# Performance work log

Hardware: AMD Instinct MI355X
Metric: run time of the kernel (lower is better)

## Reference

```python
import jax, jax.numpy as jnp
import numpy as np

# Static multi-level feature-map shapes (H, W) per level.
SPATIAL_SHAPES = np.array([[92, 160], [46, 80], [23, 40], [12, 20]], dtype=np.int32)
NUM_HEADS = 8
NUM_LEVELS = 4
NUM_POINTS = 4      # sampling points per head per level (num_all_points)
NUM_Z = 4           # num_Z_anchors; NUM_POINTS % NUM_Z == 0
EMBED = 256
HEAD_DIM = EMBED // NUM_HEADS


def setup_inputs() -> dict:
    key = jax.random.key(0)
    ks = jax.random.split(key, 10)
    bs, nq = 2, 10000
    nv = int((SPATIAL_SHAPES[:, 0] * SPATIAL_SHAPES[:, 1]).sum())  # 19560
    query = jax.random.normal(ks[0], (bs, nq, EMBED), jnp.float32)
    value = jax.random.normal(ks[1], (bs, nv, EMBED), jnp.float32)
    query_pos = jax.random.normal(ks[2], (bs, nq, EMBED), jnp.float32)
    reference_points = jax.random.uniform(ks[3], (bs, nq, NUM_Z, 2), jnp.float32)
    W_val = jax.random.normal(ks[4], (EMBED, EMBED), jnp.float32) / jnp.sqrt(EMBED)
    b_val = jnp.zeros((EMBED,), jnp.float32)
    W_off = jax.random.normal(ks[5], (EMBED, NUM_HEADS * NUM_LEVELS * NUM_POINTS * 2), jnp.float32) * 0.01
    b_off = jax.random.normal(ks[6], (NUM_HEADS * NUM_LEVELS * NUM_POINTS * 2,), jnp.float32) * 0.5
    W_attn = jax.random.normal(ks[7], (EMBED, NUM_HEADS * NUM_LEVELS * NUM_POINTS), jnp.float32) * 0.02
    b_attn = jnp.zeros((NUM_HEADS * NUM_LEVELS * NUM_POINTS,), jnp.float32)
    spatial_shapes = jnp.asarray(SPATIAL_SHAPES)
    return {
        'query': query, 'value': value, 'query_pos': query_pos,
        'reference_points': reference_points,
        'W_val': W_val, 'b_val': b_val, 'W_off': W_off, 'b_off': b_off,
        'W_attn': W_attn, 'b_attn': b_attn, 'spatial_shapes': spatial_shapes,
    }


def _bilinear(v, x, y, H, W):
    """grid_sample(mode='bilinear', padding_mode='zeros', align_corners=False).

    v: (bs, H, W, heads, d); x, y: (bs, nq, heads, P) pixel coords.
    Returns (bs, nq, heads, P, d).
    """
    x0 = jnp.floor(x)
    y0 = jnp.floor(y)
    wx1 = x - x0
    wy1 = y - y0
    wx0 = 1.0 - wx1
    wy0 = 1.0 - wy1
    x0i = x0.astype(jnp.int32)
    y0i = y0.astype(jnp.int32)
    b = jnp.arange(v.shape[0])[:, None, None, None]
    h = jnp.arange(v.shape[3])[None, None, :, None]

    def gather(yi, xi):
        valid = (yi >= 0) & (yi < H) & (xi >= 0) & (xi < W)
        yc = jnp.clip(yi, 0, H - 1)
        xc = jnp.clip(xi, 0, W - 1)
        g = v[b, yc, xc, h]  # (bs, nq, heads, P, d)
        return g * valid[..., None].astype(v.dtype)

    return (gather(y0i, x0i) * (wy0 * wx0)[..., None]
            + gather(y0i, x0i + 1) * (wy0 * wx1)[..., None]
            + gather(y0i + 1, x0i) * (wy1 * wx0)[..., None]
            + gather(y0i + 1, x0i + 1) * (wy1 * wx1)[..., None])


def reference(query, value, query_pos, reference_points, W_val, b_val,
              W_off, b_off, W_attn, b_attn, spatial_shapes):
    bs, nq, _ = query.shape
    q = query + query_pos
    # value projection -> per-head values
    v = (value @ W_val + b_val).reshape(bs, -1, NUM_HEADS, HEAD_DIM)
    # sampling offsets and attention weights from query
    off = (q @ W_off + b_off).reshape(bs, nq, NUM_HEADS, NUM_LEVELS, NUM_POINTS, 2)
    attn = (q @ W_attn + b_attn).reshape(bs, nq, NUM_HEADS, NUM_LEVELS * NUM_POINTS)
    attn = jax.nn.softmax(attn, axis=-1).reshape(bs, nq, NUM_HEADS, NUM_LEVELS, NUM_POINTS)
    # normalize offsets by (w, h) of each level
    norm = jnp.stack([spatial_shapes[:, 1], spatial_shapes[:, 0]], -1).astype(q.dtype)  # (L, 2)
    off = off / norm[None, None, None, :, None, :]
    # fold Z-anchor reference points in, matching the shape[-1]==2 branch
    off = off.reshape(bs, nq, NUM_HEADS, NUM_LEVELS, NUM_POINTS // NUM_Z, NUM_Z, 2)
    loc = reference_points[:, :, None, None, None, :, :] + off
    loc = loc.reshape(bs, nq, NUM_HEADS, NUM_LEVELS, NUM_POINTS, 2)
    grid = 2.0 * loc - 1.0  # grid_sample convention

    start = 0
    sampled = []
    for lvl in range(NUM_LEVELS):
        H, W = int(SPATIAL_SHAPES[lvl, 0]), int(SPATIAL_SHAPES[lvl, 1])
        vl = v[:, start:start + H * W].reshape(bs, H, W, NUM_HEADS, HEAD_DIM)
        start += H * W
        # align_corners=False pixel coords
        x = ((grid[:, :, :, lvl, :, 0] + 1.0) * W - 1.0) * 0.5
        y = ((grid[:, :, :, lvl, :, 1] + 1.0) * H - 1.0) * 0.5
        sampled.append(_bilinear(vl, x, y, H, W))
    samp = jnp.stack(sampled, axis=3)  # (bs, nq, heads, L, P, d)
    out = (samp * attn[..., None]).sum(axis=(3, 4))  # (bs, nq, heads, d)
    return out.reshape(bs, nq, NUM_HEADS * HEAD_DIM)
```

## Files before the change

kernel.cpp:

```cpp
#include <hip/hip_runtime.h>
#include <hip/hip_fp16.h>

#define NQ 10000
#define BS 2
#define NV 19560
#define NH 8
#define HD 32
#define EMB 256

typedef __attribute__((ext_vector_type(8))) short bf16x8;
typedef __attribute__((ext_vector_type(8))) unsigned short u16x8;
typedef __attribute__((ext_vector_type(4))) float f32x4;
typedef __attribute__((ext_vector_type(4))) short s16x4;

__device__ __forceinline__ unsigned short f2bf(float x) {
    unsigned u = __float_as_uint(x);
    u += 0x7FFFu + ((u >> 16) & 1u);
    return (unsigned short)(u >> 16);
}

__global__ __launch_bounds__(256) void convert_W(
    const float* __restrict__ Wv, const float* __restrict__ Wo,
    const float* __restrict__ Wa, const float* __restrict__ bv,
    const float* __restrict__ bo, const float* __restrict__ ba,
    ushort* __restrict__ Bt, float* __restrict__ bias) {
    int n = blockIdx.x;
    int k = threadIdx.x;
    float x;
    if (n < 256)       x = Wv[k * 256 + n];
    else if (n < 512)  x = Wo[k * 256 + (n - 256)];
    else               x = Wa[k * 128 + (n - 512)];
    Bt[n * 256 + k] = f2bf(x);
    if (k == 0)
        bias[n] = (n < 256) ? bv[n] : (n < 512) ? bo[n - 256] : ba[n - 512];
}

__global__ __launch_bounds__(256) void gemm_fused(
    const float* __restrict__ value, const float* __restrict__ query,
    const float* __restrict__ qpos, const ushort* __restrict__ Bt,
    const float* __restrict__ bias,
    ushort* __restrict__ Cv, float* __restrict__ C0, float* __restrict__ C1)
{
    __shared__ short As[64][40], Bhs[128][40];

    const int tid = threadIdx.x;

    const int bid0 = blockIdx.x;
    int bid;
    if (bid0 < 1224) {
        bid = (bid0 & 7) * 153 + (bid0 >> 3);
    } else {
        int q = bid0 - 1224;
        int xcd = q & 7, idx = q >> 3;
        int orig = (xcd < 3) ? (xcd * 118 + idx)
                             : (3 * 118 + (xcd - 3) * 117 + idx);
        bid = 1224 + orig;
    }

    bool isval; int mblk, npan;
    if (bid < 1224) { isval = true;  mblk = bid >> 1; npan = bid & 1; }
    else { int q = bid - 1224; isval = false; mblk = q / 3; npan = q % 3; }

    const int M  = isval ? (BS * NV) : (BS * NQ);
    const int m0 = mblk * 64;
    const int n0 = npan * 128;
    const int nbase = (isval ? 0 : 256) + n0;

    const float* A = isval ? value : query;

    const int arow = tid >> 2;
    const int acol = (tid & 3) * 8;
    const bool aval = (m0 + arow) < M;
    const float* Ap  = A    + (size_t)(m0 + arow) * 256 + acol;
    const float* A2p = qpos + (size_t)(m0 + arow) * 256 + acol;
    const int brow = tid >> 1;
    const int bcol = (tid & 1) * 16;
    const ushort* Bp = Bt + (size_t)(nbase + brow) * 256 + bcol;

    const int lane = tid & 63, wave = tid >> 6;
    const int wrow = (wave >> 1) * 32, wcol = (wave & 1) * 64;
    const int lr = lane & 15, quad = lane >> 4, lk = quad * 8;

    f32x4 acc[2][4] = {};

    for (int k0 = 0; k0 < 256; k0 += 32) {
        #pragma unroll
        for (int g = 0; g < 2; g++) {
            f32x4 v = {};
            if (aval) {
                v = *(const f32x4*)(Ap + k0 + g * 4);
                if (!isval) v += *(const f32x4*)(A2p + k0 + g * 4);
            }
            s16x4 hh;
            #pragma unroll
            for (int e = 0; e < 4; e++) hh[e] = (short)f2bf(v[e]);
            *(s16x4*)&As[arow][acol + g * 4] = hh;
        }
        *(bf16x8*)&Bhs[brow][bcol]     = *(const bf16x8*)(Bp + k0);
        *(bf16x8*)&Bhs[brow][bcol + 8] = *(const bf16x8*)(Bp + k0 + 8);
        __syncthreads();

        bf16x8 af[2], bhf[4];
        #pragma unroll
        for (int i = 0; i < 2; i++)
            af[i] = *(const bf16x8*)&As[wrow + i * 16 + lr][lk];
        #pragma unroll
        for (int j = 0; j < 4; j++)
            bhf[j] = *(const bf16x8*)&Bhs[wcol + j * 16 + lr][lk];
        #pragma unroll
        for (int i = 0; i < 2; i++)
            #pragma unroll
            for (int j = 0; j < 4; j++)
                acc[i][j] = __builtin_amdgcn_mfma_f32_16x16x32_bf16(af[i], bhf[j], acc[i][j], 0, 0, 0);
        __syncthreads();
    }

    #pragma unroll
    for (int j = 0; j < 4; j++) {
        int cc = wcol + j * 16 + lr;
        int col = n0 + cc;
        float bb = bias[nbase + cc];
        #pragma unroll
        for (int i = 0; i < 2; i++) {
            int gmb = m0 + wrow + i * 16 + quad * 4;
            #pragma unroll
            for (int r = 0; r < 4; r++) {
                int gm = gmb + r;
                if (gm < M) {
                    float val = acc[i][j][r] + bb;
                    if (isval) {
                        int h = col >> 5, d = col & 31;
                        int b = (gm >= NV) ? 1 : 0;
                        int pix = gm - b * NV;
                        Cv[((size_t)(b * 8 + h) * NV + pix) * 32 + d] =
                            __half_as_ushort(__float2half(val));
                    } else {
                        if (col < 256) C0[(size_t)gm * 256 + col] = val;
                        else           C1[(size_t)gm * 128 + (col - 256)] = val;
                    }
                }
            }
        }
    }
}

__global__ __launch_bounds__(256) void sample4(
    const ushort* __restrict__ v, const float* __restrict__ off,
    const float* __restrict__ attn, const float* __restrict__ refp,
    float* __restrict__ out)
{
    __shared__ int2 s_ow[64][65];

    const int t = threadIdx.x;
    const int combo = blockIdx.x & 15;
    const int qgrp  = blockIdx.x >> 4;
    const int b  = combo & 1;
    const int h0 = combo >> 1;

    const int q = t >> 2;
    const int l = t & 3;
    const int qt = qgrp * 64 + q;
    const bool valid = qt < NQ;
    const size_t bq = (size_t)b * NQ + (valid ? qt : NQ - 1);

    {
        f32x4 lg = *(const f32x4*)(attn + bq * 128 + h0 * 16 + l * 4);
        float mx = fmaxf(fmaxf(lg[0], lg[1]), fmaxf(lg[2], lg[3]));
        mx = fmaxf(mx, __shfl_xor(mx, 1, 4));
        mx = fmaxf(mx, __shfl_xor(mx, 2, 4));
        float e0 = __expf(lg[0] - mx), e1 = __expf(lg[1] - mx);
        float e2 = __expf(lg[2] - mx), e3 = __expf(lg[3] - mx);
        float s = e0 + e1 + e2 + e3;
        s += __shfl_xor(s, 1, 4);
        s += __shfl_xor(s, 2, 4);
        float inv = 1.f / s;

        const float Wl = (l == 0) ? 160.f : (l == 1) ? 80.f : (l == 2) ? 40.f : 20.f;
        const float Hl = (l == 0) ? 92.f  : (l == 1) ? 46.f : (l == 2) ? 23.f : 12.f;
        const int  stl = (l == 0) ? 0 : (l == 1) ? 14720 : (l == 2) ? 18400 : 19320;
        const int  Wi_ = (int)Wl, Hi_ = (int)Hl;
        const int base = ((b * 8 + h0) * NV + stl) * 32;

        f32x4 of0 = *(const f32x4*)(off + bq * 256 + h0 * 32 + l * 8);
        f32x4 of1 = *(const f32x4*)(off + bq * 256 + h0 * 32 + l * 8 + 4);
        f32x4 r0  = *(const f32x4*)(refp + bq * 8);
        f32x4 r1  = *(const f32x4*)(refp + bq * 8 + 4);

        float ws[4]  = {e0 * inv, e1 * inv, e2 * inv, e3 * inv};
        float oxs[4] = {of0[0], of0[2], of1[0], of1[2]};
        float oys[4] = {of0[1], of0[3], of1[1], of1[3]};
        float rxs[4] = {r0[0], r0[2], r1[0], r1[2]};
        float rys[4] = {r0[1], r0[3], r1[1], r1[3]};

        #pragma unroll
        for (int p = 0; p < 4; p++) {
            float x = rxs[p] * Wl + oxs[p] - 0.5f;
            float y = rys[p] * Hl + oys[p] - 0.5f;
            float x0f = floorf(x), y0f = floorf(y);
            float wx1 = x - x0f, wy1 = y - y0f;
            float wx0 = 1.f - wx1, wy0 = 1.f - wy1;
            int x0 = (int)x0f, y0 = (int)y0f;
            float mx0 = ((unsigned)x0       < (unsigned)Wi_) ? 1.f : 0.f;
            float mx1 = ((unsigned)(x0 + 1) < (unsigned)Wi_) ? 1.f : 0.f;
            float my0 = ((unsigned)y0       < (unsigned)Hi_) ? 1.f : 0.f;
            float my1 = ((unsigned)(y0 + 1) < (unsigned)Hi_) ? 1.f : 0.f;
            int xc0 = min(max(x0, 0), Wi_ - 1);
            int xc1 = min(max(x0 + 1, 0), Wi_ - 1);
            int yc0 = min(max(y0, 0), Hi_ - 1);
            int yc1 = min(max(y0 + 1, 0), Hi_ - 1);
            float w = ws[p];
            int pt4 = (l * 4 + p) * 4;
            s_ow[q][pt4 + 0] = make_int2(base + (yc0 * Wi_ + xc0) * 32,
                                         __float_as_int(w * wy0 * wx0 * my0 * mx0));
            s_ow[q][pt4 + 1] = make_int2(base + (yc0 * Wi_ + xc1) * 32,
                                         __float_as_int(w * wy0 * wx1 * my0 * mx1));
            s_ow[q][pt4 + 2] = make_int2(base + (yc1 * Wi_ + xc0) * 32,
                                         __float_as_int(w * wy1 * wx0 * my1 * mx0));
            s_ow[q][pt4 + 3] = make_int2(base + (yc1 * Wi_ + xc1) * 32,
                                         __float_as_int(w * wy1 * wx1 * my1 * mx1));
        }
    }
    __syncthreads();

    const int d8 = l * 8;
    const ushort* vb = v + d8;

    float a0 = 0.f, a1 = 0.f, a2 = 0.f, a3 = 0.f;
    float a4 = 0.f, a5 = 0.f, a6 = 0.f, a7 = 0.f;

    #pragma unroll
    for (int bt = 0; bt < 8; bt++) {
        int2 ow[8];
        #pragma unroll
        for (int pp = 0; pp < 2; pp++)
            #pragma unroll
            for (int c = 0; c < 4; c++)
                ow[pp * 4 + c] = s_ow[q][(bt * 2 + pp) * 4 + c];

        u16x8 u[8];
        #pragma unroll
        for (int i = 0; i < 8; i++)
            u[i] = *(const u16x8*)(vb + ow[i].x);

        #pragma unroll
        for (int i = 0; i < 8; i++) {
            float w = __int_as_float(ow[i].y);
            const __half2* hp = (const __half2*)&u[i];
            float2 f0 = __half22float2(hp[0]);
            float2 f1 = __half22float2(hp[1]);
            float2 f2 = __half22float2(hp[2]);
            float2 f3 = __half22float2(hp[3]);
            a0 += w * f0.x; a1 += w * f0.y;
            a2 += w * f1.x; a3 += w * f1.y;
            a4 += w * f2.x; a5 += w * f2.y;
            a6 += w * f3.x; a7 += w * f3.y;
        }
    }

    if (valid) {
        float* op = out + bq * 256 + h0 * 32 + d8;
        f32x4 o0 = {a0, a1, a2, a3}, o1 = {a4, a5, a6, a7};
        *(f32x4*)op       = o0;
        *(f32x4*)(op + 4) = o1;
    }
}

extern "C" void kernel_launch(void* const* d_in, const int* in_sizes, int n_in,
                              void* d_out, int out_size, void* d_ws, size_t ws_size,
                              hipStream_t stream) {
    const float* query     = (const float*)d_in[0];
    const float* value     = (const float*)d_in[1];
    const float* query_pos = (const float*)d_in[2];
    const float* refp      = (const float*)d_in[3];
    const float* W_val     = (const float*)d_in[4];
    const float* b_val     = (const float*)d_in[5];
    const float* W_off     = (const float*)d_in[6];
    const float* b_off     = (const float*)d_in[7];
    const float* W_attn    = (const float*)d_in[8];
    const float* b_attn    = (const float*)d_in[9];
    float* out = (float*)d_out;

    char* w = (char*)d_ws;
    float*  off    = (float*)w;   w += 20480000;
    float*  attn   = (float*)w;   w += 10240000;
    ushort* vp_bf  = (ushort*)w;  w += 20029440;
    ushort* Bt     = (ushort*)w;  w += 327680;
    float*  bias_c = (float*)w;   w += 2560;

    convert_W<<<640, 256, 0, stream>>>(W_val, W_off, W_attn, b_val, b_off, b_attn,
                                       Bt, bias_c);

    gemm_fused<<<1224 + 939, 256, 0, stream>>>(value, query, query_pos, Bt, bias_c,
                                               vp_bf, off, attn);

    sample4<<<157 * 16, 256, 0, stream>>>(vp_bf, off, attn, refp, out);
}
```

Measured before the change: 199.8 us.

## Split fused GEMM into value and query kernels; batch 16 gathers in sampler

The single fused projection GEMM is split into two specialised kernels, one for the value projection and one for the query projection. This removes the per-block isval branching and the separate block-index remapping paths. The sampling kernel now loads 16 gather offsets and issues 16 vector loads per batch instead of 8, using byte offsets, to keep more memory requests in flight. The trade-offs are an extra kernel launch, losing overlap between the two GEMMs in one grid, and higher register pressure in the sampler.

```diff
diff --git a/kernel.cpp b/kernel.cpp
--- a/kernel.cpp
+++ b/kernel.cpp
@@ -35,44 +35,113 @@
         bias[n] = (n < 256) ? bv[n] : (n < 512) ? bo[n - 256] : ba[n - 512];
 }
 
-__global__ __launch_bounds__(256) void gemm_fused(
-    const float* __restrict__ value, const float* __restrict__ query,
-    const float* __restrict__ qpos, const ushort* __restrict__ Bt,
-    const float* __restrict__ bias,
-    ushort* __restrict__ Cv, float* __restrict__ C0, float* __restrict__ C1)
+__global__ __launch_bounds__(256) void gemm_val(
+    const float* __restrict__ value, const ushort* __restrict__ Bt,
+    const float* __restrict__ bias, ushort* __restrict__ Cv)
 {
     __shared__ short As[64][40], Bhs[128][40];
 
     const int tid = threadIdx.x;
 
     const int bid0 = blockIdx.x;
-    int bid;
-    if (bid0 < 1224) {
-        bid = (bid0 & 7) * 153 + (bid0 >> 3);
-    } else {
-        int q = bid0 - 1224;
-        int xcd = q & 7, idx = q >> 3;
-        int orig = (xcd < 3) ? (xcd * 118 + idx)
-                             : (3 * 118 + (xcd - 3) * 117 + idx);
-        bid = 1224 + orig;
-    }
-
-    bool isval; int mblk, npan;
-    if (bid < 1224) { isval = true;  mblk = bid >> 1; npan = bid & 1; }
-    else { int q = bid - 1224; isval = false; mblk = q / 3; npan = q % 3; }
-
-    const int M  = isval ? (BS * NV) : (BS * NQ);
+    const int bid = (bid0 & 7) * 153 + (bid0 >> 3);
+
+    const int mblk = bid >> 1, npan = bid & 1;
+    const int M  = BS * NV;
     const int m0 = mblk * 64;
     const int n0 = npan * 128;
-    const int nbase = (isval ? 0 : 256) + n0;
-
-    const float* A = isval ? value : query;
 
     const int arow = tid >> 2;
     const int acol = (tid & 3) * 8;
     const bool aval = (m0 + arow) < M;
-    const float* Ap  = A    + (size_t)(m0 + arow) * 256 + acol;
-    const float* A2p = qpos + (size_t)(m0 + arow) * 256 + acol;
+    const float* Ap = value + (size_t)(m0 + arow) * 256 + acol;
+    const int brow = tid >> 1;
+    const int bcol = (tid & 1) * 16;
+    const ushort* Bp = Bt + (size_t)(n0 + brow) * 256 + bcol;
+
+    const int lane = tid & 63, wave = tid >> 6;
+    const int wrow = (wave >> 1) * 32, wcol = (wave & 1) * 64;
+    const int lr = lane & 15, quad = lane >> 4, lk = quad * 8;
+
+    f32x4 acc[2][4] = {};
+
+    for (int k0 = 0; k0 < 256; k0 += 32) {
+        #pragma unroll
+        for (int g = 0; g < 2; g++) {
+            f32x4 v = {};
+            if (aval) v = *(const f32x4*)(Ap + k0 + g * 4);
+            s16x4 hh;
+            #pragma unroll
+            for (int e = 0; e < 4; e++) hh[e] = (short)f2bf(v[e]);
+            *(s16x4*)&As[arow][acol + g * 4] = hh;
+        }
+        *(bf16x8*)&Bhs[brow][bcol]     = *(const bf16x8*)(Bp + k0);
+        *(bf16x8*)&Bhs[brow][bcol + 8] = *(const bf16x8*)(Bp + k0 + 8);
+        __syncthreads();
+
+        bf16x8 af[2], bhf[4];
+        #pragma unroll
+        for (int i = 0; i < 2; i++)
+            af[i] = *(const bf16x8*)&As[wrow + i * 16 + lr][lk];
+        #pragma unroll
+        for (int j = 0; j < 4; j++)
+            bhf[j] = *(const bf16x8*)&Bhs[wcol + j * 16 + lr][lk];
+        #pragma unroll
+        for (int i = 0; i < 2; i++)
+            #pragma unroll
+            for (int j = 0; j < 4; j++)
+                acc[i][j] = __builtin_amdgcn_mfma_f32_16x16x32_bf16(af[i], bhf[j], acc[i][j], 0, 0, 0);
+        __syncthreads();
+    }
+
+    #pragma unroll
+    for (int j = 0; j < 4; j++) {
+        int col = n0 + wcol + j * 16 + lr;
+        float bb = bias[col];
+        int h = col >> 5, d = col & 31;
+        #pragma unroll
+        for (int i = 0; i < 2; i++) {
+            int gmb = m0 + wrow + i * 16 + quad * 4;
+            #pragma unroll
+            for (int r = 0; r < 4; r++) {
+                int gm = gmb + r;
+                if (gm < M) {
+                    float val = acc[i][j][r] + bb;
+                    int b = (gm >= NV) ? 1 : 0;
+                    int pix = gm - b * NV;
+                    Cv[((size_t)(b * 8 + h) * NV + pix) * 32 + d] =
+                        __half_as_ushort(__float2half(val));
+                }
+            }
+        }
+    }
+}
+
+__global__ __launch_bounds__(256) void gemm_query(
+    const float* __restrict__ query, const float* __restrict__ qpos,
+    const ushort* __restrict__ Bt, const float* __restrict__ bias,
+    float* __restrict__ C0, float* __restrict__ C1)
+{
+    __shared__ short As[64][40], Bhs[128][40];
+
+    const int tid = threadIdx.x;
+
+    const int q0 = blockIdx.x;
+    const int xcd = q0 & 7, idx = q0 >> 3;
+    const int bid = (xcd < 3) ? (xcd * 118 + idx)
+                              : (3 * 118 + (xcd - 3) * 117 + idx);
+
+    const int mblk = bid / 3, npan = bid % 3;
+    const int M  = BS * NQ;
+    const int m0 = mblk * 64;
+    const int n0 = npan * 128;
+    const int nbase = 256 + n0;
+
+    const int arow = tid >> 2;
+    const int acol = (tid & 3) * 8;
+    const bool aval = (m0 + arow) < M;
+    const float* Ap  = query + (size_t)(m0 + arow) * 256 + acol;
+    const float* A2p = qpos  + (size_t)(m0 + arow) * 256 + acol;
     const int brow = tid >> 1;
     const int bcol = (tid & 1) * 16;
     const ushort* Bp = Bt + (size_t)(nbase + brow) * 256 + bcol;
@@ -89,7 +158,7 @@
             f32x4 v = {};
             if (aval) {
                 v = *(const f32x4*)(Ap + k0 + g * 4);
-                if (!isval) v += *(const f32x4*)(A2p + k0 + g * 4);
+                v += *(const f32x4*)(A2p + k0 + g * 4);
             }
             s16x4 hh;
             #pragma unroll
@@ -128,16 +197,8 @@
                 int gm = gmb + r;
                 if (gm < M) {
                     float val = acc[i][j][r] + bb;
-                    if (isval) {
-                        int h = col >> 5, d = col & 31;
-                        int b = (gm >= NV) ? 1 : 0;
-                        int pix = gm - b * NV;
-                        Cv[((size_t)(b * 8 + h) * NV + pix) * 32 + d] =
-                            __half_as_ushort(__float2half(val));
-                    } else {
-                        if (col < 256) C0[(size_t)gm * 256 + col] = val;
-                        else           C1[(size_t)gm * 128 + (col - 256)] = val;
-                    }
+                    if (col < 256) C0[(size_t)gm * 256 + col] = val;
+                    else           C1[(size_t)gm * 128 + (col - 256)] = val;
                 }
             }
         }
@@ -179,7 +240,7 @@
         const float Hl = (l == 0) ? 92.f  : (l == 1) ? 46.f : (l == 2) ? 23.f : 12.f;
         const int  stl = (l == 0) ? 0 : (l == 1) ? 14720 : (l == 2) ? 18400 : 19320;
         const int  Wi_ = (int)Wl, Hi_ = (int)Hl;
-        const int base = ((b * 8 + h0) * NV + stl) * 32;
+        const int base = ((b * 8 + h0) * NV + stl) * 64;
 
         f32x4 of0 = *(const f32x4*)(off + bq * 256 + h0 * 32 + l * 8);
         f32x4 of1 = *(const f32x4*)(off + bq * 256 + h0 * 32 + l * 8 + 4);
@@ -210,40 +271,37 @@
             int yc1 = min(max(y0 + 1, 0), Hi_ - 1);
             float w = ws[p];
             int pt4 = (l * 4 + p) * 4;
-            s_ow[q][pt4 + 0] = make_int2(base + (yc0 * Wi_ + xc0) * 32,
+            s_ow[q][pt4 + 0] = make_int2(base + (yc0 * Wi_ + xc0) * 64,
                                          __float_as_int(w * wy0 * wx0 * my0 * mx0));
-            s_ow[q][pt4 + 1] = make_int2(base + (yc0 * Wi_ + xc1) * 32,
+            s_ow[q][pt4 + 1] = make_int2(base + (yc0 * Wi_ + xc1) * 64,
                                          __float_as_int(w * wy0 * wx1 * my0 * mx1));
-            s_ow[q][pt4 + 2] = make_int2(base + (yc1 * Wi_ + xc0) * 32,
+            s_ow[q][pt4 + 2] = make_int2(base + (yc1 * Wi_ + xc0) * 64,
                                          __float_as_int(w * wy1 * wx0 * my1 * mx0));
-            s_ow[q][pt4 + 3] = make_int2(base + (yc1 * Wi_ + xc1) * 32,
+            s_ow[q][pt4 + 3] = make_int2(base + (yc1 * Wi_ + xc1) * 64,
                                          __float_as_int(w * wy1 * wx1 * my1 * mx1));
         }
     }
     __syncthreads();
 
-    const int d8 = l * 8;
-    const ushort* vb = v + d8;
+    const char* vb = (const char*)v + l * 16;
 
     float a0 = 0.f, a1 = 0.f, a2 = 0.f, a3 = 0.f;
     float a4 = 0.f, a5 = 0.f, a6 = 0.f, a7 = 0.f;
 
     #pragma unroll
-    for (int bt = 0; bt < 8; bt++) {
-        int2 ow[8];
-        #pragma unroll
-        for (int pp = 0; pp < 2; pp++)
-            #pragma unroll
-            for (int c = 0; c < 4; c++)
-                ow[pp * 4 + c] = s_ow[q][(bt * 2 + pp) * 4 + c];
-
-        u16x8 u[8];
-        #pragma unroll
-        for (int i = 0; i < 8; i++)
+    for (int ib = 0; ib < 4; ib++) {
+        int2 ow[16];
+        #pragma unroll
+        for (int c = 0; c < 16; c++)
+            ow[c] = s_ow[q][ib * 16 + c];
+
+        u16x8 u[16];
+        #pragma unroll
+        for (int i = 0; i < 16; i++)
             u[i] = *(const u16x8*)(vb + ow[i].x);
 
         #pragma unroll
-        for (int i = 0; i < 8; i++) {
+        for (int i = 0; i < 16; i++) {
             float w = __int_as_float(ow[i].y);
             const __half2* hp = (const __half2*)&u[i];
             float2 f0 = __half22float2(hp[0]);
@@ -258,7 +316,7 @@
     }
 
     if (valid) {
-        float* op = out + bq * 256 + h0 * 32 + d8;
+        float* op = out + bq * 256 + h0 * 32 + l * 8;
         f32x4 o0 = {a0, a1, a2, a3}, o1 = {a4, a5, a6, a7};
         *(f32x4*)op       = o0;
         *(f32x4*)(op + 4) = o1;
@@ -290,8 +348,8 @@
     convert_W<<<640, 256, 0, stream>>>(W_val, W_off, W_attn, b_val, b_off, b_attn,
                                        Bt, bias_c);
 
-    gemm_fused<<<1224 + 939, 256, 0, stream>>>(value, query, query_pos, Bt, bias_c,
-                                               vp_bf, off, attn);
+    gemm_val<<<1224, 256, 0, stream>>>(value, Bt, bias_c, vp_bf);
+    gemm_query<<<939, 256, 0, stream>>>(query, query_pos, Bt, bias_c, off, attn);
 
     sample4<<<157 * 16, 256, 0, stream>>>(vp_bf, off, attn, refp, out);
 }
```

New measurement: 203.0 us. No clear change (+1.6%).

## Pack sampling offsets compactly and double-buffer value gathers in sampler

Applied to the files above, without the earlier changes.

The sampler now stores one packed 32-bit word per sampling point (base pixel index plus x/y neighbour deltas) and one float4 of corner weights, replacing four int2 entries per point. This cuts LDS footprint and shared-memory reads. The gather loop is restructured into an explicit two-buffer schedule that issues the next batch of value loads before the current FMAs, to overlap memory latency with compute. Launch bounds request 4 blocks per CU, which may limit registers given the doubled load buffers.

```diff
diff --git a/kernel.cpp b/kernel.cpp
--- a/kernel.cpp
+++ b/kernel.cpp
@@ -144,12 +144,13 @@
     }
 }
 
-__global__ __launch_bounds__(256) void sample4(
+__global__ __launch_bounds__(256, 4) void sample4(
     const ushort* __restrict__ v, const float* __restrict__ off,
     const float* __restrict__ attn, const float* __restrict__ refp,
     float* __restrict__ out)
 {
-    __shared__ int2 s_ow[64][65];
+    __shared__ unsigned s_o[64][17];
+    __shared__ f32x4    s_w[64][17];
 
     const int t = threadIdx.x;
     const int combo = blockIdx.x & 15;
@@ -179,7 +180,7 @@
         const float Hl = (l == 0) ? 92.f  : (l == 1) ? 46.f : (l == 2) ? 23.f : 12.f;
         const int  stl = (l == 0) ? 0 : (l == 1) ? 14720 : (l == 2) ? 18400 : 19320;
         const int  Wi_ = (int)Wl, Hi_ = (int)Hl;
-        const int base = ((b * 8 + h0) * NV + stl) * 32;
+        const int base = (b * 8 + h0) * NV + stl;
 
         f32x4 of0 = *(const f32x4*)(off + bq * 256 + h0 * 32 + l * 8);
         f32x4 of1 = *(const f32x4*)(off + bq * 256 + h0 * 32 + l * 8 + 4);
@@ -209,56 +210,81 @@
             int yc0 = min(max(y0, 0), Hi_ - 1);
             int yc1 = min(max(y0 + 1, 0), Hi_ - 1);
             float w = ws[p];
-            int pt4 = (l * 4 + p) * 4;
-            s_ow[q][pt4 + 0] = make_int2(base + (yc0 * Wi_ + xc0) * 32,
-                                         __float_as_int(w * wy0 * wx0 * my0 * mx0));
-            s_ow[q][pt4 + 1] = make_int2(base + (yc0 * Wi_ + xc1) * 32,
-                                         __float_as_int(w * wy0 * wx1 * my0 * mx1));
-            s_ow[q][pt4 + 2] = make_int2(base + (yc1 * Wi_ + xc0) * 32,
-                                         __float_as_int(w * wy1 * wx0 * my1 * mx0));
-            s_ow[q][pt4 + 3] = make_int2(base + (yc1 * Wi_ + xc1) * 32,
-                                         __float_as_int(w * wy1 * wx1 * my1 * mx1));
+            int pt = l * 4 + p;
+            unsigned off0 = (unsigned)(base + yc0 * Wi_ + xc0);
+            unsigned dxf  = (unsigned)(xc1 - xc0);
+            unsigned dyW  = (unsigned)((yc1 - yc0) * Wi_);
+            s_o[q][pt] = off0 | (dxf << 19) | (dyW << 20);
+            f32x4 wv = {w * wy0 * wx0 * my0 * mx0,
+                        w * wy0 * wx1 * my0 * mx1,
+                        w * wy1 * wx0 * my1 * mx0,
+                        w * wy1 * wx1 * my1 * mx1};
+            s_w[q][pt] = wv;
         }
     }
     __syncthreads();
 
-    const int d8 = l * 8;
-    const ushort* vb = v + d8;
+    const char* vb = (const char*)v + l * 16;
 
     float a0 = 0.f, a1 = 0.f, a2 = 0.f, a3 = 0.f;
     float a4 = 0.f, a5 = 0.f, a6 = 0.f, a7 = 0.f;
 
-    #pragma unroll
-    for (int bt = 0; bt < 8; bt++) {
-        int2 ow[8];
-        #pragma unroll
-        for (int pp = 0; pp < 2; pp++)
-            #pragma unroll
-            for (int c = 0; c < 4; c++)
-                ow[pp * 4 + c] = s_ow[q][(bt * 2 + pp) * 4 + c];
-
-        u16x8 u[8];
-        #pragma unroll
-        for (int i = 0; i < 8; i++)
-            u[i] = *(const u16x8*)(vb + ow[i].x);
-
-        #pragma unroll
-        for (int i = 0; i < 8; i++) {
-            float w = __int_as_float(ow[i].y);
-            const __half2* hp = (const __half2*)&u[i];
-            float2 f0 = __half22float2(hp[0]);
-            float2 f1 = __half22float2(hp[1]);
-            float2 f2 = __half22float2(hp[2]);
-            float2 f3 = __half22float2(hp[3]);
-            a0 += w * f0.x; a1 += w * f0.y;
-            a2 += w * f1.x; a3 += w * f1.y;
-            a4 += w * f2.x; a5 += w * f2.y;
-            a6 += w * f3.x; a7 += w * f3.y;
-        }
-    }
+#define LOADB(d, k) { \
+    unsigned ua = s_o[q][(k) * 2], ub = s_o[q][(k) * 2 + 1]; \
+    int oa = (int)(ua & 0x7FFFFu) << 6; \
+    int dxa = (int)((ua >> 19) & 1u) << 6; \
+    int dya = (int)(ua >> 20) << 6; \
+    int ob = (int)(ub & 0x7FFFFu) << 6; \
+    int dxb = (int)((ub >> 19) & 1u) << 6; \
+    int dyb = (int)(ub >> 20) << 6; \
+    d[0] = *(const u16x8*)(vb + oa); \
+    d[1] = *(const u16x8*)(vb + oa + dxa); \
+    d[2] = *(const u16x8*)(vb + oa + dya); \
+    d[3] = *(const u16x8*)(vb + oa + dxa + dya); \
+    d[4] = *(const u16x8*)(vb + ob); \
+    d[5] = *(const u16x8*)(vb + ob + dxb); \
+    d[6] = *(const u16x8*)(vb + ob + dyb); \
+    d[7] = *(const u16x8*)(vb + ob + dxb + dyb); }
+
+#define FMAB(d, k) { \
+    f32x4 wa = s_w[q][(k) * 2], wb = s_w[q][(k) * 2 + 1]; \
+    _Pragma("unroll") \
+    for (int i = 0; i < 8; i++) { \
+        float w = (i < 4) ? wa[i] : wb[i - 4]; \
+        const __half2* hp = (const __half2*)&d[i]; \
+        float2 f0 = __half22float2(hp[0]); \
+        float2 f1 = __half22float2(hp[1]); \
+        float2 f2 = __half22float2(hp[2]); \
+        float2 f3 = __half22float2(hp[3]); \
+        a0 += w * f0.x; a1 += w * f0.y; \
+        a2 += w * f1.x; a3 += w * f1.y; \
+        a4 += w * f2.x; a5 += w * f2.y; \
+        a6 += w * f3.x; a7 += w * f3.y; } }
+
+    {
+        u16x8 dA[8], dB[8];
+        LOADB(dA, 0);
+        LOADB(dB, 1);
+        FMAB(dA, 0);
+        LOADB(dA, 2);
+        FMAB(dB, 1);
+        LOADB(dB, 3);
+        FMAB(dA, 2);
+        LOADB(dA, 4);
+        FMAB(dB, 3);
+        LOADB(dB, 5);
+        FMAB(dA, 4);
+        LOADB(dA, 6);
+        FMAB(dB, 5);
+        LOADB(dB, 7);
+        FMAB(dA, 6);
+        FMAB(dB, 7);
+    }
+#undef LOADB
+#undef FMAB
 
     if (valid) {
-        float* op = out + bq * 256 + h0 * 32 + d8;
+        float* op = out + bq * 256 + h0 * 32 + l * 8;
         f32x4 o0 = {a0, a1, a2, a3}, o1 = {a4, a5, a6, a7};
         *(f32x4*)op       = o0;
         *(f32x4*)(op + 4) = o1;
```

Measured after the change: 202.1 us. About the same (+1.2%).
